# Optimization experiments

Measured on AMD Instinct MI355X. Metric: run time of the kernel, lower is better.

## Reference

```python
import jax, jax.numpy as jnp
import numpy as np

B, T, TREF, C, H = 2, 2048, 512, 768, 12
D = C // H


def setup_inputs() -> dict:
    key = jax.random.key(0)
    ks = jax.random.split(key, 20)
    s = 0.02  # init scale for weights
    inp = {
        "x": jax.random.normal(ks[0], (B, T, C), dtype=jnp.float32),
        "mask": jax.random.randint(ks[1], (B, 1, T, T), 0, 2, dtype=jnp.int32),
        "rel_pos": jax.random.normal(ks[2], (H, T, T), dtype=jnp.float32) * 0.1,
        "ref_feat": jax.random.normal(ks[3], (B, TREF, C), dtype=jnp.float32),
    }
    names = ["Wq", "Wk", "Wv", "Wrk", "Wrv", "Wo"]
    for i, n in enumerate(names):
        inp[n] = jax.random.normal(ks[4 + i], (C, C), dtype=jnp.float32) * s
        inp["b" + n[1:]] = jnp.zeros((C,), dtype=jnp.float32)
    return inp


def _heads(t, W, b):
    # nn.Linear: y = t @ W.T + b, then (B, L, H, D) -> (B, H, L, D)
    Bt, L, _ = t.shape
    return (t @ W.T + b).reshape(Bt, L, H, D).transpose(0, 2, 1, 3)


def reference(x, mask, rel_pos, ref_feat, Wq, bq, Wk, bk, Wv, bv,
              Wrk, brk, Wrv, brv, Wo, bo):
    Bx, Tx, Cx = x.shape
    Tref = ref_feat.shape[1]
    q = _heads(x, Wq, bq)                  # (B,H,T,D)
    k = _heads(x, Wk, bk)
    v = _heads(x, Wv, bv)
    rk = _heads(ref_feat, Wrk, brk)        # (B,H,Tref,D)
    rv = _heads(ref_feat, Wrv, brv)
    k = jnp.concatenate([k, rk], axis=2)   # (B,H,T+Tref,D)
    v = jnp.concatenate([v, rv], axis=2)
    # additive bias: -inf where mask==1 (self keys), rel_pos on self keys,
    # ref keys get 0 bias (mask padded with 0)
    bias_self = jnp.where(mask == 1, -jnp.inf, 0.0).astype(x.dtype) + rel_pos[None]  # (B,H,T,T)
    bias = jnp.pad(bias_self, ((0, 0), (0, 0), (0, 0), (0, Tref)))  # (B,H,T,T+Tref)
    scale = 1.0 / jnp.sqrt(jnp.asarray(D, dtype=x.dtype))
    scores = jnp.einsum('bhqd,bhkd->bhqk', q, k) * scale + bias
    attn = jax.nn.softmax(scores, axis=-1)
    y = jnp.einsum('bhqk,bhkd->bhqd', attn, v)
    y = y.transpose(0, 2, 1, 3).reshape(Bx, Tx, Cx)
    return y @ Wo.T + bo
```

## Files before the change

### kernel.cpp

```cpp
#include <hip/hip_runtime.h>


typedef __bf16 bf16x8 __attribute__((ext_vector_type(8)));
typedef float floatx4 __attribute__((ext_vector_type(4)));

__device__ __forceinline__ ushort f2bf(float f) {
  uint u = __builtin_bit_cast(uint, f);
  return (ushort)((u + 0x7FFFu + ((u >> 16) & 1u)) >> 16);
}

__global__ __launch_bounds__(256) void cast_all(
    const float* __restrict__ x, const float* __restrict__ rf,
    const float* __restrict__ w0, const float* __restrict__ w1,
    const float* __restrict__ w2, const float* __restrict__ w3,
    const float* __restrict__ w4, const float* __restrict__ w5,
    ushort* __restrict__ dst) {
  size_t i4 = ((size_t)blockIdx.x * 256 + threadIdx.x) * 4;
  const float* src;
  size_t off;
  if (i4 < 3145728) { src = x; off = i4; }
  else if (i4 < 3932160) { src = rf; off = i4 - 3145728; }
  else {
    size_t r = i4 - 3932160;
    if (r < 589824) { src = w0; off = r; }
    else if (r < 2 * 589824) { src = w1; off = r - 589824; }
    else if (r < 3 * 589824) { src = w2; off = r - 2 * 589824; }
    else if (r < 4 * 589824) { src = w3; off = r - 3 * 589824; }
    else if (r < 5 * 589824) { src = w4; off = r - 4 * 589824; }
    else { src = w5; off = r - 5 * 589824; }
  }
  float4 v = *(const float4*)(src + off);
  ushort4 o;
  o.x = f2bf(v.x); o.y = f2bf(v.y); o.z = f2bf(v.z); o.w = f2bf(v.w);
  *(ushort4*)(dst + i4) = o;
}

__device__ __forceinline__ void gemm_core(
    const ushort* __restrict__ Ab, const ushort* __restrict__ Bb,
    ushort* As, ushort* Bs, int tid, int quad, int l16, int mw, int nw,
    floatx4 acc[4][4]) {
  const int r0 = tid >> 2, kp = (tid & 3) * 8;
  const int r1 = r0 + 64;
#pragma unroll 1
  for (int kb = 0; kb < 24; ++kb) {
    const int k0 = kb * 32;
    uint4 av0 = *(const uint4*)(Ab + (size_t)r0 * 768 + k0 + kp);
    uint4 av1 = *(const uint4*)(Ab + (size_t)r1 * 768 + k0 + kp);
    uint4 bv0 = *(const uint4*)(Bb + (size_t)r0 * 768 + k0 + kp);
    uint4 bv1 = *(const uint4*)(Bb + (size_t)r1 * 768 + k0 + kp);
    __syncthreads();
    *(uint4*)&As[tid * 8] = av0;
    *(uint4*)&As[(tid + 256) * 8] = av1;
    *(uint4*)&Bs[tid * 8] = bv0;
    *(uint4*)&Bs[(tid + 256) * 8] = bv1;
    __syncthreads();
    bf16x8 af[4], bfr[4];
#pragma unroll
    for (int mt = 0; mt < 4; ++mt)
      af[mt] = *(const bf16x8*)&As[(mw + mt * 16 + l16) * 32 + quad * 8];
#pragma unroll
    for (int nt = 0; nt < 4; ++nt)
      bfr[nt] = *(const bf16x8*)&Bs[(nw + nt * 16 + l16) * 32 + quad * 8];
#pragma unroll
    for (int mt = 0; mt < 4; ++mt)
#pragma unroll
      for (int nt = 0; nt < 4; ++nt)
        acc[mt][nt] = __builtin_amdgcn_mfma_f32_16x16x32_bf16(af[mt], bfr[nt], acc[mt][nt], 0, 0, 0);
  }
}

template <int REF>
__global__ __launch_bounds__(256) void gemm_fused(
    const ushort* __restrict__ A, const ushort* __restrict__ W,
    const float* __restrict__ bA, const float* __restrict__ bB,
    const float* __restrict__ bC,
    ushort* __restrict__ oA, ushort* __restrict__ oB, ushort* __restrict__ oC) {
  const int bm = blockIdx.x, bn = blockIdx.y;
  const int tid = threadIdx.x;
  const int w = tid >> 6, lane = tid & 63, quad = lane >> 4, l16 = lane & 15;
  const int mw = (w >> 1) * 64, nw = (w & 1) * 64;

  __shared__ __align__(16) ushort As[128 * 32];
  __shared__ __align__(16) ushort Bs[128 * 32];

  floatx4 acc[4][4];
#pragma unroll
  for (int mt = 0; mt < 4; ++mt)
#pragma unroll
    for (int nt = 0; nt < 4; ++nt) acc[mt][nt] = (floatx4){0.f, 0.f, 0.f, 0.f};

  gemm_core(A + (size_t)bm * 128 * 768, W + (size_t)bn * 128 * 768,
            As, Bs, tid, quad, l16, mw, nw, acc);

  const int sec = bn / 6;
  const float* bp = sec == 0 ? bA : sec == 1 ? bB : bC;
  ushort* op = sec == 0 ? oA : sec == 1 ? oB : oC;
  const bool qlay = (REF == 0 && sec == 0);
#pragma unroll
  for (int nt = 0; nt < 4; ++nt) {
    const int nloc = (bn - sec * 6) * 128 + nw + nt * 16 + l16;
    const float bv = bp[nloc];
    const int hh = nloc >> 6, dd = nloc & 63;
#pragma unroll
    for (int mt = 0; mt < 4; ++mt)
#pragma unroll
      for (int i = 0; i < 4; ++i) {
        const int m = bm * 128 + mw + mt * 16 + quad * 4 + i;
        int bb, tt;
        if (REF == 0) { bb = m >> 11; tt = m & 2047; }
        else { bb = m >> 9; tt = (m & 511) + 2048; }
        const size_t idx = qlay ? (((size_t)(bb * 12 + hh) * 2048 + tt) * 64 + dd)
                                : (((size_t)(bb * 12 + hh) * 2560 + tt) * 64 + dd);
        op[idx] = f2bf(acc[mt][nt][i] + bv);
      }
  }
}

__global__ __launch_bounds__(256) void gemm_out(
    const ushort* __restrict__ A, const ushort* __restrict__ W,
    const float* __restrict__ bias, float* __restrict__ out) {
  const int bm = blockIdx.x, bn = blockIdx.y;
  const int tid = threadIdx.x;
  const int w = tid >> 6, lane = tid & 63, quad = lane >> 4, l16 = lane & 15;
  const int mw = (w >> 1) * 64, nw = (w & 1) * 64;

  __shared__ __align__(16) ushort As[128 * 32];
  __shared__ __align__(16) ushort Bs[128 * 32];

  floatx4 acc[4][4];
#pragma unroll
  for (int mt = 0; mt < 4; ++mt)
#pragma unroll
    for (int nt = 0; nt < 4; ++nt) acc[mt][nt] = (floatx4){0.f, 0.f, 0.f, 0.f};

  gemm_core(A + (size_t)bm * 128 * 768, W + (size_t)bn * 128 * 768,
            As, Bs, tid, quad, l16, mw, nw, acc);

#pragma unroll
  for (int nt = 0; nt < 4; ++nt) {
    const int n = bn * 128 + nw + nt * 16 + l16;
    const float bv = bias[n];
#pragma unroll
    for (int mt = 0; mt < 4; ++mt)
#pragma unroll
      for (int i = 0; i < 4; ++i) {
        const int m = bm * 128 + mw + mt * 16 + quad * 4 + i;
        out[(size_t)m * 768 + n] = acc[mt][nt][i] + bv;
      }
  }
}

__global__ __launch_bounds__(256, 3) void attn(
    const ushort* __restrict__ qb, const ushort* __restrict__ kb,
    const ushort* __restrict__ vb, const int* __restrict__ mask,
    const float* __restrict__ relp, ushort* __restrict__ yb) {
  const int b = blockIdx.x, qt = blockIdx.y, h = blockIdx.z;
  const int tid = threadIdx.x;
  const int w = tid >> 6, lane = tid & 63, quad = lane >> 4, l16 = lane & 15;

  __shared__ __align__(16) ushort Qs[64 * 72];
  __shared__ __align__(16) ushort Ks[64 * 72];
  __shared__ __align__(16) ushort Vs[64 * 64];
  __shared__ __align__(16) ushort Ps[4][16 * 72];
  __shared__ float BiasS[64 * 65];

  const ushort* qsrc = qb + ((size_t)(b * 12 + h) * 2048 + qt * 64) * 64;
  const ushort* ksrc = kb + (size_t)(b * 12 + h) * 2560 * 64;
  const ushort* vsrc = vb + (size_t)(b * 12 + h) * 2560 * 64;
  const int* mbase = mask + ((size_t)b * 2048 + qt * 64) * 2048;
  const float* rbase = relp + ((size_t)h * 2048 + qt * 64) * 2048;

#pragma unroll
  for (int c = 0; c < 2; ++c) {
    const int f = tid + c * 256;
    *(uint4*)&Qs[(f >> 3) * 72 + (f & 7) * 8] = *(const uint4*)(qsrc + f * 8);
  }

  uint4 kd[2], vd[2];
  int4 md[4];
  float4 rd[4];
  {
    kd[0] = *(const uint4*)(ksrc + tid * 8);
    kd[1] = *(const uint4*)(ksrc + (tid + 256) * 8);
    vd[0] = *(const uint4*)(vsrc + tid * 8);
    vd[1] = *(const uint4*)(vsrc + (tid + 256) * 8);
#pragma unroll
    for (int p = 0; p < 4; ++p) {
      const int f2 = tid * 4 + p * 1024, row = f2 >> 6, col = f2 & 63;
      md[p] = *(const int4*)(mbase + (size_t)row * 2048 + col);
      rd[p] = *(const float4*)(rbase + (size_t)row * 2048 + col);
    }
  }
  __syncthreads();

#pragma unroll
  for (int c = 0; c < 2; ++c) {
    const int f = tid + c * 256;
    *(uint4*)&Ks[(f >> 3) * 72 + (f & 7) * 8] = kd[c];
    const int key = f >> 3, d0 = (f & 7) * 8;
    const int cb = (((key >> 3) ^ (f & 7)) & 7) * 8 + (key & 7);
    uint vv[4] = {vd[c].x, vd[c].y, vd[c].z, vd[c].w};
#pragma unroll
    for (int u = 0; u < 4; ++u) {
      Vs[(d0 + 2 * u) * 64 + cb] = (ushort)(vv[u] & 0xffffu);
      Vs[(d0 + 2 * u + 1) * 64 + cb] = (ushort)(vv[u] >> 16);
    }
  }
#pragma unroll
  for (int p = 0; p < 4; ++p) {
    const int f2 = tid * 4 + p * 1024, row = f2 >> 6, col = f2 & 63;
    float* bsw = &BiasS[row * 65 + col];
    bsw[0] = md[p].x ? -__builtin_inff() : rd[p].x;
    bsw[1] = md[p].y ? -__builtin_inff() : rd[p].y;
    bsw[2] = md[p].z ? -__builtin_inff() : rd[p].z;
    bsw[3] = md[p].w ? -__builtin_inff() : rd[p].w;
  }

  bf16x8 bQ[2];
  bQ[0] = *(const bf16x8*)&Qs[(w * 16 + l16) * 72 + quad * 8];
  bQ[1] = *(const bf16x8*)&Qs[(w * 16 + l16) * 72 + 32 + quad * 8];

  floatx4 acc[4];
#pragma unroll
  for (int mt = 0; mt < 4; ++mt) acc[mt] = (floatx4){0.f, 0.f, 0.f, 0.f};
  float m_run = -__builtin_inff(), l_run = 0.f;

  __syncthreads();

#pragma unroll 1
  for (int kt = 0; kt < 40; ++kt) {
    const int ktn = kt + 1;
    if (ktn < 40) {
      const ushort* kt0 = ksrc + ktn * 4096;
      const ushort* vt0 = vsrc + ktn * 4096;
      kd[0] = *(const uint4*)(kt0 + tid * 8);
      kd[1] = *(const uint4*)(kt0 + (tid + 256) * 8);
      vd[0] = *(const uint4*)(vt0 + tid * 8);
      vd[1] = *(const uint4*)(vt0 + (tid + 256) * 8);
      if (ktn < 32) {
#pragma unroll
        for (int p = 0; p < 4; ++p) {
          const int f2 = tid * 4 + p * 1024, row = f2 >> 6, col = f2 & 63;
          md[p] = *(const int4*)(mbase + (size_t)row * 2048 + ktn * 64 + col);
          rd[p] = *(const float4*)(rbase + (size_t)row * 2048 + ktn * 64 + col);
        }
      }
    }

    float s[16];
    {
      floatx4 st[4];
#pragma unroll
      for (int mt = 0; mt < 4; ++mt) st[mt] = (floatx4){0.f, 0.f, 0.f, 0.f};
#pragma unroll
      for (int kk = 0; kk < 2; ++kk) {
#pragma unroll
        for (int mt = 0; mt < 4; ++mt) {
          bf16x8 aK = *(const bf16x8*)&Ks[(mt * 16 + l16) * 72 + kk * 32 + quad * 8];
          st[mt] = __builtin_amdgcn_mfma_f32_16x16x32_bf16(aK, bQ[kk], st[mt], 0, 0, 0);
        }
      }
#pragma unroll
      for (int mt = 0; mt < 4; ++mt)
#pragma unroll
        for (int i = 0; i < 4; ++i) s[mt * 4 + i] = st[mt][i] * 0.125f;
    }

    if (kt < 32) {
      const float* brow = &BiasS[(w * 16 + l16) * 65 + quad * 4];
#pragma unroll
      for (int mt = 0; mt < 4; ++mt)
#pragma unroll
        for (int i = 0; i < 4; ++i) s[mt * 4 + i] += brow[mt * 16 + i];
    }

    float tm = s[0];
#pragma unroll
    for (int j = 1; j < 16; ++j) tm = fmaxf(tm, s[j]);
    tm = fmaxf(tm, __shfl_xor(tm, 16));
    tm = fmaxf(tm, __shfl_xor(tm, 32));
    const float mnew = fmaxf(m_run, tm);
    const float mref = (mnew == -__builtin_inff()) ? 0.f : mnew;
    const float alpha = (m_run == -__builtin_inff()) ? 0.f : __expf(m_run - mnew);
    float p[16], rs = 0.f;
#pragma unroll
    for (int j = 0; j < 16; ++j) { p[j] = __expf(s[j] - mref); rs += p[j]; }
    rs += __shfl_xor(rs, 16);
    rs += __shfl_xor(rs, 32);
    l_run = l_run * alpha + rs;
    m_run = mnew;
#pragma unroll
    for (int mt = 0; mt < 4; ++mt)
#pragma unroll
      for (int i = 0; i < 4; ++i) acc[mt][i] *= alpha;

    ushort* pw = &Ps[w][l16 * 72 + quad * 4];
#pragma unroll
    for (int mt = 0; mt < 4; ++mt) {
      const uint pk0 = (uint)f2bf(p[mt * 4 + 0]) | ((uint)f2bf(p[mt * 4 + 1]) << 16);
      const uint pk1 = (uint)f2bf(p[mt * 4 + 2]) | ((uint)f2bf(p[mt * 4 + 3]) << 16);
      *(uint*)&pw[mt * 16] = pk0;
      *(uint*)&pw[mt * 16 + 2] = pk1;
    }

#pragma unroll
    for (int kk = 0; kk < 2; ++kk) {
      const bf16x8 bP = *(const bf16x8*)&Ps[w][l16 * 72 + kk * 32 + quad * 8];
#pragma unroll
      for (int mt = 0; mt < 4; ++mt) {
        const int dd = mt * 16 + l16;
        const int cs = (((kk * 4 + quad) ^ (dd >> 3)) & 7) * 8;
        const bf16x8 aV = *(const bf16x8*)&Vs[dd * 64 + cs];
        acc[mt] = __builtin_amdgcn_mfma_f32_16x16x32_bf16(aV, bP, acc[mt], 0, 0, 0);
      }
    }

    __syncthreads();

    if (ktn < 40) {
#pragma unroll
      for (int c = 0; c < 2; ++c) {
        const int f = tid + c * 256;
        *(uint4*)&Ks[(f >> 3) * 72 + (f & 7) * 8] = kd[c];
        const int key = f >> 3, d0 = (f & 7) * 8;
        const int cb = (((key >> 3) ^ (f & 7)) & 7) * 8 + (key & 7);
        uint vv[4] = {vd[c].x, vd[c].y, vd[c].z, vd[c].w};
#pragma unroll
        for (int u = 0; u < 4; ++u) {
          Vs[(d0 + 2 * u) * 64 + cb] = (ushort)(vv[u] & 0xffffu);
          Vs[(d0 + 2 * u + 1) * 64 + cb] = (ushort)(vv[u] >> 16);
        }
      }
      if (ktn < 32) {
#pragma unroll
        for (int p = 0; p < 4; ++p) {
          const int f2 = tid * 4 + p * 1024, row = f2 >> 6, col = f2 & 63;
          float* bsw = &BiasS[row * 65 + col];
          bsw[0] = md[p].x ? -__builtin_inff() : rd[p].x;
          bsw[1] = md[p].y ? -__builtin_inff() : rd[p].y;
          bsw[2] = md[p].z ? -__builtin_inff() : rd[p].z;
          bsw[3] = md[p].w ? -__builtin_inff() : rd[p].w;
        }
      }
    }
    __syncthreads();
  }

  const float inv = 1.f / l_run;
  ushort* yrow = yb + ((size_t)b * 2048 + qt * 64 + w * 16 + l16) * 768 + h * 64;
#pragma unroll
  for (int mt = 0; mt < 4; ++mt)
#pragma unroll
    for (int i = 0; i < 4; ++i)
      yrow[mt * 16 + quad * 4 + i] = f2bf(acc[mt][i] * inv);
}

extern "C" void kernel_launch(void* const* d_in, const int* in_sizes, int n_in,
                              void* d_out, int out_size, void* d_ws, size_t ws_size,
                              hipStream_t stream) {
  const float* x = (const float*)d_in[0];
  const int* mask = (const int*)d_in[1];
  const float* relp = (const float*)d_in[2];
  const float* ref = (const float*)d_in[3];
  const float* Wq = (const float*)d_in[4];
  const float* bq = (const float*)d_in[5];
  const float* Wk = (const float*)d_in[6];
  const float* bk = (const float*)d_in[7];
  const float* Wv = (const float*)d_in[8];
  const float* bv = (const float*)d_in[9];
  const float* Wrk = (const float*)d_in[10];
  const float* brk = (const float*)d_in[11];
  const float* Wrv = (const float*)d_in[12];
  const float* brv = (const float*)d_in[13];
  const float* Wo = (const float*)d_in[14];
  const float* bo = (const float*)d_in[15];

  ushort* xb = (ushort*)d_ws;
  ushort* refb = xb + 3145728;
  ushort* wb = refb + 786432;
  ushort* qbuf = wb + 6 * 589824;
  ushort* kbuf = qbuf + 3145728;
  ushort* vbuf = kbuf + 3932160;
  ushort* ybuf = vbuf + 3932160;

  cast_all<<<7296, 256, 0, stream>>>(x, ref, Wq, Wk, Wv, Wrk, Wrv, Wo, xb);

  gemm_fused<0><<<dim3(32, 18), 256, 0, stream>>>(
      xb, wb, bq, bk, bv, qbuf, kbuf, vbuf);
  gemm_fused<1><<<dim3(8, 12), 256, 0, stream>>>(
      refb, wb + (size_t)3 * 589824, brk, brv, nullptr, kbuf, vbuf, nullptr);

  attn<<<dim3(2, 32, 12), 256, 0, stream>>>(qbuf, kbuf, vbuf, mask, relp, ybuf);

  gemm_out<<<dim3(32, 6), 256, 0, stream>>>(
      ybuf, wb + (size_t)5 * 589824, bo, (float*)d_out);
}
```

Before: 527.2 us.

## Bit-pack mask, widen attention key tile, and use direct global-to-LDS GEMM loads

Adds a pre-pass that packs the int32 mask into 64-bit bitmasks, so attention reads far fewer mask bytes than it did when it read the int mask once per head. The attention kernel now works on 128-key tiles, stores rel_pos as bf16 in shared memory, applies the mask bits in registers, and reuses the bias buffer for P. This removes the fp32 bias LDS staging and halves the number of loop iterations and barriers. The GEMM core switches to global_load_lds for direct global-to-shared copies. Risks are bf16 rounding of rel_pos, higher register pressure from the 8-wide score tile, and extra barriers in the GEMM.

```diff
diff --git a/kernel.cpp b/kernel.cpp
--- a/kernel.cpp
+++ b/kernel.cpp
@@ -7,6 +7,15 @@
 __device__ __forceinline__ ushort f2bf(float f) {
   uint u = __builtin_bit_cast(uint, f);
   return (ushort)((u + 0x7FFFu + ((u >> 16) & 1u)) >> 16);
+}
+__device__ __forceinline__ float bf2f(ushort u) {
+  return __builtin_bit_cast(float, (uint)u << 16);
+}
+
+__device__ __forceinline__ void gld16(ushort* lds, const ushort* g) {
+  __builtin_amdgcn_global_load_lds(
+      (const __attribute__((address_space(1))) unsigned int*)g,
+      (__attribute__((address_space(3))) unsigned int*)lds, 16, 0, 0);
 }
 
 __global__ __launch_bounds__(256) void cast_all(
@@ -35,24 +44,40 @@
   *(ushort4*)(dst + i4) = o;
 }
 
+__global__ __launch_bounds__(256) void pack_mask(
+    const int* __restrict__ mask, unsigned long long* __restrict__ bits) {
+  const int gid = blockIdx.x * 256 + threadIdx.x;
+  const int4* src = (const int4*)(mask + (size_t)gid * 64);
+  unsigned long long v = 0;
+#pragma unroll
+  for (int j = 0; j < 16; ++j) {
+    int4 m = src[j];
+    unsigned long long nib = (m.x ? 1ull : 0ull) | (m.y ? 2ull : 0ull) |
+                             (m.z ? 4ull : 0ull) | (m.w ? 8ull : 0ull);
+    v |= nib << (j * 4);
+  }
+  bits[gid] = v;
+}
+
 __device__ __forceinline__ void gemm_core(
     const ushort* __restrict__ Ab, const ushort* __restrict__ Bb,
     ushort* As, ushort* Bs, int tid, int quad, int l16, int mw, int nw,
     floatx4 acc[4][4]) {
+  const int w = tid >> 6;
   const int r0 = tid >> 2, kp = (tid & 3) * 8;
-  const int r1 = r0 + 64;
+  const size_t ga0 = (size_t)r0 * 768 + kp;
+  const size_t ga1 = ga0 + (size_t)64 * 768;
+  ushort* lA0 = &As[w * 512];
+  ushort* lA1 = &As[w * 512 + 2048];
+  ushort* lB0 = &Bs[w * 512];
+  ushort* lB1 = &Bs[w * 512 + 2048];
 #pragma unroll 1
   for (int kb = 0; kb < 24; ++kb) {
     const int k0 = kb * 32;
-    uint4 av0 = *(const uint4*)(Ab + (size_t)r0 * 768 + k0 + kp);
-    uint4 av1 = *(const uint4*)(Ab + (size_t)r1 * 768 + k0 + kp);
-    uint4 bv0 = *(const uint4*)(Bb + (size_t)r0 * 768 + k0 + kp);
-    uint4 bv1 = *(const uint4*)(Bb + (size_t)r1 * 768 + k0 + kp);
-    __syncthreads();
-    *(uint4*)&As[tid * 8] = av0;
-    *(uint4*)&As[(tid + 256) * 8] = av1;
-    *(uint4*)&Bs[tid * 8] = bv0;
-    *(uint4*)&Bs[(tid + 256) * 8] = bv1;
+    gld16(lA0, Ab + ga0 + k0);
+    gld16(lA1, Ab + ga1 + k0);
+    gld16(lB0, Bb + ga0 + k0);
+    gld16(lB1, Bb + ga1 + k0);
     __syncthreads();
     bf16x8 af[4], bfr[4];
 #pragma unroll
@@ -66,6 +91,7 @@
 #pragma unroll
       for (int nt = 0; nt < 4; ++nt)
         acc[mt][nt] = __builtin_amdgcn_mfma_f32_16x16x32_bf16(af[mt], bfr[nt], acc[mt][nt], 0, 0, 0);
+    __syncthreads();
   }
 }
 
@@ -152,139 +178,151 @@
 
 __global__ __launch_bounds__(256, 3) void attn(
     const ushort* __restrict__ qb, const ushort* __restrict__ kb,
-    const ushort* __restrict__ vb, const int* __restrict__ mask,
+    const ushort* __restrict__ vb, const unsigned long long* __restrict__ bits,
     const float* __restrict__ relp, ushort* __restrict__ yb) {
   const int b = blockIdx.x, qt = blockIdx.y, h = blockIdx.z;
   const int tid = threadIdx.x;
   const int w = tid >> 6, lane = tid & 63, quad = lane >> 4, l16 = lane & 15;
 
-  __shared__ __align__(16) ushort Qs[64 * 72];
-  __shared__ __align__(16) ushort Ks[64 * 72];
-  __shared__ __align__(16) ushort Vs[64 * 64];
-  __shared__ __align__(16) ushort Ps[4][16 * 72];
-  __shared__ float BiasS[64 * 65];
+  __shared__ __align__(16) ushort Ks[128 * 72];
+  __shared__ __align__(16) ushort Vs[64 * 128];
+  __shared__ __align__(16) ushort RPs[64 * 136];
 
   const ushort* qsrc = qb + ((size_t)(b * 12 + h) * 2048 + qt * 64) * 64;
   const ushort* ksrc = kb + (size_t)(b * 12 + h) * 2560 * 64;
   const ushort* vsrc = vb + (size_t)(b * 12 + h) * 2560 * 64;
-  const int* mbase = mask + ((size_t)b * 2048 + qt * 64) * 2048;
+  const int qrow = qt * 64 + w * 16 + l16;
+  const unsigned long long* brow = bits + ((size_t)b * 2048 + qrow) * 32;
   const float* rbase = relp + ((size_t)h * 2048 + qt * 64) * 2048;
 
 #pragma unroll
   for (int c = 0; c < 2; ++c) {
     const int f = tid + c * 256;
-    *(uint4*)&Qs[(f >> 3) * 72 + (f & 7) * 8] = *(const uint4*)(qsrc + f * 8);
-  }
-
-  uint4 kd[2], vd[2];
-  int4 md[4];
-  float4 rd[4];
+    *(uint4*)&Ks[(f >> 3) * 72 + (f & 7) * 8] = *(const uint4*)(qsrc + f * 8);
+  }
+  uint4 kreg[4], vreg[4];
+  float4 rreg[8];
+  ulonglong2 breg;
   {
-    kd[0] = *(const uint4*)(ksrc + tid * 8);
-    kd[1] = *(const uint4*)(ksrc + (tid + 256) * 8);
-    vd[0] = *(const uint4*)(vsrc + tid * 8);
-    vd[1] = *(const uint4*)(vsrc + (tid + 256) * 8);
-#pragma unroll
-    for (int p = 0; p < 4; ++p) {
-      const int f2 = tid * 4 + p * 1024, row = f2 >> 6, col = f2 & 63;
-      md[p] = *(const int4*)(mbase + (size_t)row * 2048 + col);
-      rd[p] = *(const float4*)(rbase + (size_t)row * 2048 + col);
-    }
+#pragma unroll
+    for (int c = 0; c < 4; ++c) {
+      const int f = tid + c * 256;
+      kreg[c] = *(const uint4*)(ksrc + f * 8);
+      vreg[c] = *(const uint4*)(vsrc + f * 8);
+    }
+#pragma unroll
+    for (int p = 0; p < 8; ++p) {
+      const int f4 = tid + p * 256, row = f4 >> 5, c4 = f4 & 31;
+      rreg[p] = *(const float4*)(rbase + (size_t)row * 2048 + c4 * 4);
+    }
+    breg = *(const ulonglong2*)brow;
   }
   __syncthreads();
-
-#pragma unroll
-  for (int c = 0; c < 2; ++c) {
-    const int f = tid + c * 256;
-    *(uint4*)&Ks[(f >> 3) * 72 + (f & 7) * 8] = kd[c];
-    const int key = f >> 3, d0 = (f & 7) * 8;
-    const int cb = (((key >> 3) ^ (f & 7)) & 7) * 8 + (key & 7);
-    uint vv[4] = {vd[c].x, vd[c].y, vd[c].z, vd[c].w};
-#pragma unroll
-    for (int u = 0; u < 4; ++u) {
-      Vs[(d0 + 2 * u) * 64 + cb] = (ushort)(vv[u] & 0xffffu);
-      Vs[(d0 + 2 * u + 1) * 64 + cb] = (ushort)(vv[u] >> 16);
-    }
-  }
-#pragma unroll
-  for (int p = 0; p < 4; ++p) {
-    const int f2 = tid * 4 + p * 1024, row = f2 >> 6, col = f2 & 63;
-    float* bsw = &BiasS[row * 65 + col];
-    bsw[0] = md[p].x ? -__builtin_inff() : rd[p].x;
-    bsw[1] = md[p].y ? -__builtin_inff() : rd[p].y;
-    bsw[2] = md[p].z ? -__builtin_inff() : rd[p].z;
-    bsw[3] = md[p].w ? -__builtin_inff() : rd[p].w;
-  }
-
   bf16x8 bQ[2];
-  bQ[0] = *(const bf16x8*)&Qs[(w * 16 + l16) * 72 + quad * 8];
-  bQ[1] = *(const bf16x8*)&Qs[(w * 16 + l16) * 72 + 32 + quad * 8];
+  bQ[0] = *(const bf16x8*)&Ks[(w * 16 + l16) * 72 + quad * 8];
+  bQ[1] = *(const bf16x8*)&Ks[(w * 16 + l16) * 72 + 32 + quad * 8];
 
   floatx4 acc[4];
 #pragma unroll
   for (int mt = 0; mt < 4; ++mt) acc[mt] = (floatx4){0.f, 0.f, 0.f, 0.f};
   float m_run = -__builtin_inff(), l_run = 0.f;
 
-  __syncthreads();
-
 #pragma unroll 1
-  for (int kt = 0; kt < 40; ++kt) {
-    const int ktn = kt + 1;
-    if (ktn < 40) {
-      const ushort* kt0 = ksrc + ktn * 4096;
-      const ushort* vt0 = vsrc + ktn * 4096;
-      kd[0] = *(const uint4*)(kt0 + tid * 8);
-      kd[1] = *(const uint4*)(kt0 + (tid + 256) * 8);
-      vd[0] = *(const uint4*)(vt0 + tid * 8);
-      vd[1] = *(const uint4*)(vt0 + (tid + 256) * 8);
-      if (ktn < 32) {
-#pragma unroll
-        for (int p = 0; p < 4; ++p) {
-          const int f2 = tid * 4 + p * 1024, row = f2 >> 6, col = f2 & 63;
-          md[p] = *(const int4*)(mbase + (size_t)row * 2048 + ktn * 64 + col);
-          rd[p] = *(const float4*)(rbase + (size_t)row * 2048 + ktn * 64 + col);
+  for (int it = 0; it < 20; ++it) {
+    const bool self = it < 16;
+    __syncthreads();
+#pragma unroll
+    for (int c = 0; c < 4; ++c) {
+      const int f = tid + c * 256;
+      *(uint4*)&Ks[(f >> 3) * 72 + (f & 7) * 8] = kreg[c];
+      const int key = f >> 3, d0 = (f & 7) * 8;
+      const int kh = key & 63, half = key >> 6;
+      const int col = half * 64 + (((kh >> 3) ^ (f & 7)) & 7) * 8 + (kh & 7);
+      uint vv[4] = {vreg[c].x, vreg[c].y, vreg[c].z, vreg[c].w};
+#pragma unroll
+      for (int u = 0; u < 4; ++u) {
+        Vs[(d0 + 2 * u) * 128 + col] = (ushort)(vv[u] & 0xffffu);
+        Vs[(d0 + 2 * u + 1) * 128 + col] = (ushort)(vv[u] >> 16);
+      }
+    }
+    if (self) {
+#pragma unroll
+      for (int p = 0; p < 8; ++p) {
+        const int f4 = tid + p * 256, row = f4 >> 5, c4 = f4 & 31;
+        uint2 pk;
+        pk.x = (uint)f2bf(rreg[p].x) | ((uint)f2bf(rreg[p].y) << 16);
+        pk.y = (uint)f2bf(rreg[p].z) | ((uint)f2bf(rreg[p].w) << 16);
+        *(uint2*)&RPs[row * 136 + c4 * 4] = pk;
+      }
+    }
+    __syncthreads();
+    const ulonglong2 bcur = breg;
+    const int itn = it + 1;
+    if (itn < 20) {
+      const ushort* kt0 = ksrc + itn * 8192;
+      const ushort* vt0 = vsrc + itn * 8192;
+#pragma unroll
+      for (int c = 0; c < 4; ++c) {
+        const int f = tid + c * 256;
+        kreg[c] = *(const uint4*)(kt0 + f * 8);
+        vreg[c] = *(const uint4*)(vt0 + f * 8);
+      }
+      if (itn < 16) {
+#pragma unroll
+        for (int p = 0; p < 8; ++p) {
+          const int f4 = tid + p * 256, row = f4 >> 5, c4 = f4 & 31;
+          rreg[p] = *(const float4*)(rbase + (size_t)row * 2048 + itn * 128 + c4 * 4);
         }
-      }
-    }
-
-    float s[16];
-    {
-      floatx4 st[4];
-#pragma unroll
-      for (int mt = 0; mt < 4; ++mt) st[mt] = (floatx4){0.f, 0.f, 0.f, 0.f};
-#pragma unroll
-      for (int kk = 0; kk < 2; ++kk) {
-#pragma unroll
-        for (int mt = 0; mt < 4; ++mt) {
-          bf16x8 aK = *(const bf16x8*)&Ks[(mt * 16 + l16) * 72 + kk * 32 + quad * 8];
-          st[mt] = __builtin_amdgcn_mfma_f32_16x16x32_bf16(aK, bQ[kk], st[mt], 0, 0, 0);
+        breg = *(const ulonglong2*)(brow + itn * 2);
+      }
+    }
+
+    floatx4 st[8];
+#pragma unroll
+    for (int mt = 0; mt < 8; ++mt) st[mt] = (floatx4){0.f, 0.f, 0.f, 0.f};
+#pragma unroll
+    for (int kk = 0; kk < 2; ++kk)
+#pragma unroll
+      for (int mt = 0; mt < 8; ++mt) {
+        bf16x8 aK = *(const bf16x8*)&Ks[(mt * 16 + l16) * 72 + kk * 32 + quad * 8];
+        st[mt] = __builtin_amdgcn_mfma_f32_16x16x32_bf16(aK, bQ[kk], st[mt], 0, 0, 0);
+      }
+#pragma unroll
+    for (int mt = 0; mt < 8; ++mt) {
+      if (self) {
+        const ushort4 rv4 = *(const ushort4*)&RPs[(w * 16 + l16) * 136 + mt * 16 + quad * 4];
+        const ushort rv[4] = {rv4.x, rv4.y, rv4.z, rv4.w};
+        const unsigned long long word = (mt < 4) ? bcur.x : bcur.y;
+#pragma unroll
+        for (int i = 0; i < 4; ++i) {
+          float sv = st[mt][i] * 0.125f + bf2f(rv[i]);
+          const int bit = (mt & 3) * 16 + quad * 4 + i;
+          st[mt][i] = ((word >> bit) & 1ull) ? -__builtin_inff() : sv;
         }
-      }
-#pragma unroll
-      for (int mt = 0; mt < 4; ++mt)
-#pragma unroll
-        for (int i = 0; i < 4; ++i) s[mt * 4 + i] = st[mt][i] * 0.125f;
-    }
-
-    if (kt < 32) {
-      const float* brow = &BiasS[(w * 16 + l16) * 65 + quad * 4];
-#pragma unroll
-      for (int mt = 0; mt < 4; ++mt)
-#pragma unroll
-        for (int i = 0; i < 4; ++i) s[mt * 4 + i] += brow[mt * 16 + i];
-    }
-
-    float tm = s[0];
-#pragma unroll
-    for (int j = 1; j < 16; ++j) tm = fmaxf(tm, s[j]);
+      } else {
+#pragma unroll
+        for (int i = 0; i < 4; ++i) st[mt][i] *= 0.125f;
+      }
+    }
+    float tm = st[0][0];
+#pragma unroll
+    for (int mt = 0; mt < 8; ++mt)
+#pragma unroll
+      for (int i = 0; i < 4; ++i) tm = fmaxf(tm, st[mt][i]);
     tm = fmaxf(tm, __shfl_xor(tm, 16));
     tm = fmaxf(tm, __shfl_xor(tm, 32));
     const float mnew = fmaxf(m_run, tm);
     const float mref = (mnew == -__builtin_inff()) ? 0.f : mnew;
     const float alpha = (m_run == -__builtin_inff()) ? 0.f : __expf(m_run - mnew);
-    float p[16], rs = 0.f;
-#pragma unroll
-    for (int j = 0; j < 16; ++j) { p[j] = __expf(s[j] - mref); rs += p[j]; }
+    float rs = 0.f;
+#pragma unroll
+    for (int mt = 0; mt < 8; ++mt)
+#pragma unroll
+      for (int i = 0; i < 4; ++i) {
+        const float pv = __expf(st[mt][i] - mref);
+        st[mt][i] = pv;
+        rs += pv;
+      }
     rs += __shfl_xor(rs, 16);
     rs += __shfl_xor(rs, 32);
     l_run = l_run * alpha + rs;
@@ -294,56 +332,27 @@
 #pragma unroll
       for (int i = 0; i < 4; ++i) acc[mt][i] *= alpha;
 
-    ushort* pw = &Ps[w][l16 * 72 + quad * 4];
-#pragma unroll
-    for (int mt = 0; mt < 4; ++mt) {
-      const uint pk0 = (uint)f2bf(p[mt * 4 + 0]) | ((uint)f2bf(p[mt * 4 + 1]) << 16);
-      const uint pk1 = (uint)f2bf(p[mt * 4 + 2]) | ((uint)f2bf(p[mt * 4 + 3]) << 16);
-      *(uint*)&pw[mt * 16] = pk0;
-      *(uint*)&pw[mt * 16 + 2] = pk1;
-    }
-
-#pragma unroll
-    for (int kk = 0; kk < 2; ++kk) {
-      const bf16x8 bP = *(const bf16x8*)&Ps[w][l16 * 72 + kk * 32 + quad * 8];
+    {
+      ushort* pw = &RPs[(w * 16 + l16) * 136];
+#pragma unroll
+      for (int mt = 0; mt < 8; ++mt) {
+        uint2 pk;
+        pk.x = (uint)f2bf(st[mt][0]) | ((uint)f2bf(st[mt][1]) << 16);
+        pk.y = (uint)f2bf(st[mt][2]) | ((uint)f2bf(st[mt][3]) << 16);
+        *(uint2*)&pw[mt * 16 + quad * 4] = pk;
+      }
+    }
+#pragma unroll
+    for (int kk = 0; kk < 4; ++kk) {
+      const bf16x8 bP = *(const bf16x8*)&RPs[(w * 16 + l16) * 136 + kk * 32 + quad * 8];
 #pragma unroll
       for (int mt = 0; mt < 4; ++mt) {
         const int dd = mt * 16 + l16;
-        const int cs = (((kk * 4 + quad) ^ (dd >> 3)) & 7) * 8;
-        const bf16x8 aV = *(const bf16x8*)&Vs[dd * 64 + cs];
+        const int cs = ((((kk & 1) * 4 + quad) ^ (dd >> 3)) & 7) * 8;
+        const bf16x8 aV = *(const bf16x8*)&Vs[dd * 128 + (kk >> 1) * 64 + cs];
         acc[mt] = __builtin_amdgcn_mfma_f32_16x16x32_bf16(aV, bP, acc[mt], 0, 0, 0);
       }
     }
-
-    __syncthreads();
-
-    if (ktn < 40) {
-#pragma unroll
-      for (int c = 0; c < 2; ++c) {
-        const int f = tid + c * 256;
-        *(uint4*)&Ks[(f >> 3) * 72 + (f & 7) * 8] = kd[c];
-        const int key = f >> 3, d0 = (f & 7) * 8;
-        const int cb = (((key >> 3) ^ (f & 7)) & 7) * 8 + (key & 7);
-        uint vv[4] = {vd[c].x, vd[c].y, vd[c].z, vd[c].w};
-#pragma unroll
-        for (int u = 0; u < 4; ++u) {
-          Vs[(d0 + 2 * u) * 64 + cb] = (ushort)(vv[u] & 0xffffu);
-          Vs[(d0 + 2 * u + 1) * 64 + cb] = (ushort)(vv[u] >> 16);
-        }
-      }
-      if (ktn < 32) {
-#pragma unroll
-        for (int p = 0; p < 4; ++p) {
-          const int f2 = tid * 4 + p * 1024, row = f2 >> 6, col = f2 & 63;
-          float* bsw = &BiasS[row * 65 + col];
-          bsw[0] = md[p].x ? -__builtin_inff() : rd[p].x;
-          bsw[1] = md[p].y ? -__builtin_inff() : rd[p].y;
-          bsw[2] = md[p].z ? -__builtin_inff() : rd[p].z;
-          bsw[3] = md[p].w ? -__builtin_inff() : rd[p].w;
-        }
-      }
-    }
-    __syncthreads();
   }
 
   const float inv = 1.f / l_run;
@@ -382,15 +391,17 @@
   ushort* kbuf = qbuf + 3145728;
   ushort* vbuf = kbuf + 3932160;
   ushort* ybuf = vbuf + 3932160;
+  unsigned long long* bitsbuf = (unsigned long long*)(ybuf + 3145728);
 
   cast_all<<<7296, 256, 0, stream>>>(x, ref, Wq, Wk, Wv, Wrk, Wrv, Wo, xb);
+  pack_mask<<<512, 256, 0, stream>>>(mask, bitsbuf);
 
   gemm_fused<0><<<dim3(32, 18), 256, 0, stream>>>(
       xb, wb, bq, bk, bv, qbuf, kbuf, vbuf);
   gemm_fused<1><<<dim3(8, 12), 256, 0, stream>>>(
       refb, wb + (size_t)3 * 589824, brk, brv, nullptr, kbuf, vbuf, nullptr);
 
-  attn<<<dim3(2, 32, 12), 256, 0, stream>>>(qbuf, kbuf, vbuf, mask, relp, ybuf);
+  attn<<<dim3(2, 32, 12), 256, 0, stream>>>(qbuf, kbuf, vbuf, bitsbuf, relp, ybuf);
 
   gemm_out<<<dim3(32, 6), 256, 0, stream>>>(
       ybuf, wb + (size_t)5 * 589824, bo, (float*)d_out);
```

New measurement: 711.8 us. 35.0% more time.
